# Kernel tuning notes

Hardware: AMD Instinct MI355X
Metric: run time of the kernel (lower is better)

The kernel has to match this reference:

```python
import jax, jax.numpy as jnp
import numpy as np

D_OUT = 512          # full_tensor_dims[0]
VIEW_DIMS = (512, 512, 512)
RANK = 32
BATCH = 4096


def _xavier(key, shape):
    # xavier-style init: scale by sqrt(2 / (fan_in + fan_out)) over first/last dims
    fan_in, fan_out = shape[0] * shape[1], shape[2]
    scale = jnp.sqrt(2.0 / (fan_in + fan_out)).astype(jnp.float32)
    return jax.random.normal(key, shape, dtype=jnp.float32) * scale


def setup_inputs() -> dict:
    key = jax.random.key(0)
    ks = jax.random.split(key, 8)
    X0 = jax.random.normal(ks[0], (VIEW_DIMS[0], BATCH), dtype=jnp.float32)
    X1 = jax.random.normal(ks[1], (VIEW_DIMS[1], BATCH), dtype=jnp.float32)
    X2 = jax.random.normal(ks[2], (VIEW_DIMS[2], BATCH), dtype=jnp.float32)
    # TT cores: rank chain [1, 32, 32, 32, 1]
    core0 = _xavier(ks[3], (1, D_OUT, RANK))            # [1, d_out, r1]
    core1 = _xavier(ks[4], (RANK, VIEW_DIMS[0], RANK))  # [r1, d1, r2]
    core2 = _xavier(ks[5], (RANK, VIEW_DIMS[1], RANK))  # [r2, d2, r3]
    core3 = _xavier(ks[6], (RANK, VIEW_DIMS[2], 1))     # [r3, d3, 1]
    return {"X0": X0, "X1": X1, "X2": X2,
            "core0": core0, "core1": core1, "core2": core2, "core3": core3}


def reference(X0, X1, X2, core0, core1, core2, core3):
    # Batched equivalent of the per-sample Python loop in TensorTrain.forward.
    # For each view j: M_j[n] = mode_dot(core_{j+1}^T_{0,2,1}, X_j[:, n], mode=2)
    #   == einsum('adb,dn->nab'), shape [B, r_{j+1}, r_{j+2}]
    Xs = (X0, X1, X2)
    chain_cores = (core1, core2, core3)
    Ms = [jnp.einsum('adb,dn->nab', c, x) for c, x in zip(chain_cores, Xs)]
    # Chain of per-sample matmuls: z = M_0 @ M_1 @ M_2 -> [B, r1, 1]
    acc = Ms[0]
    for M in Ms[1:]:
        acc = jnp.einsum('nab,nbc->nac', acc, M)
    # Z[:, n] = mode_dot(core0, z[:, 0], mode=2)[0, :]
    Z = jnp.einsum('oda,na->dn', core0, acc[:, :, 0])  # [d_out, B]
    return Z


if __name__ == '__main__':
    out = reference(**setup_inputs())
    print(out.shape)
```

## Files before the change

### kernel.cpp

```cpp
#include <hip/hip_runtime.h>

#define D 512
#define B 4096
#define R 32
#define AB 1024

typedef unsigned short ushort_t;
typedef __attribute__((ext_vector_type(8))) short bf16x8;
typedef __attribute__((ext_vector_type(4))) float f32x4;

__device__ __forceinline__ ushort_t f2bf(float f) {
  uint32_t u = __builtin_bit_cast(uint32_t, f);
  u = (u + 0x7FFFu + ((u >> 16) & 1u)) >> 16;
  return (ushort_t)u;
}
__device__ __forceinline__ float bf2f(ushort_t h) {
  uint32_t u = ((uint32_t)h) << 16;
  return __builtin_bit_cast(float, u);
}
__device__ __forceinline__ void gload_lds16(const void* g, void* lds) {
  __builtin_amdgcn_global_load_lds(
      (const __attribute__((address_space(1))) unsigned int*)g,
      (__attribute__((address_space(3))) unsigned int*)lds, 16, 0, 0);
}

__global__ __launch_bounds__(256) void pack_cores(
    const float* __restrict__ c1, const float* __restrict__ c2,
    ushort_t* __restrict__ Apack)
{
  __shared__ ushort_t T[R][D + 8];
  const int ja = blockIdx.x, j = ja >> 5, a = ja & 31;
  const float* __restrict__ c = j ? c2 : c1;
  const int tid = threadIdx.x;
#pragma unroll
  for (int i = 0; i < 64; ++i) {
    int e = i * 256 + tid;
    T[e & 31][e >> 5] = f2bf(c[(size_t)a * (D * R) + e]);
  }
  __syncthreads();
#pragma unroll
  for (int i = 0; i < 8; ++i) {
    int ch = i * 256 + tid;
    int b = ch >> 6, off = (ch & 63) * 8;
    ushort_t v[8];
#pragma unroll
    for (int q = 0; q < 8; ++q) v[q] = T[b][off + q];
    *(bf16x8*)&Apack[((size_t)j * AB + a * 32 + b) * D + off] = *(bf16x8*)v;
  }
}

__global__ __launch_bounds__(256) void transpose_x(
    const float* __restrict__ X0, const float* __restrict__ X1,
    ushort_t* __restrict__ Xt)
{
  __shared__ float T[64][65];
  const int j = blockIdx.z;
  const float* __restrict__ X = j ? X1 : X0;
  ushort_t* __restrict__ O = Xt + (size_t)j * B * D;
  const int n0 = blockIdx.x * 64, d0 = blockIdx.y * 64;
  const int tid = threadIdx.x;
#pragma unroll
  for (int i = 0; i < 16; ++i) {
    int e = i * 256 + tid;
    T[e >> 6][e & 63] = X[(size_t)(d0 + (e >> 6)) * B + n0 + (e & 63)];
  }
  __syncthreads();
#pragma unroll
  for (int i = 0; i < 2; ++i) {
    int ch = i * 256 + tid;
    int nr = ch >> 3, dc = (ch & 7) * 8;
    ushort_t v[8];
#pragma unroll
    for (int q = 0; q < 8; ++q) v[q] = f2bf(T[dc + q][nr]);
    *(bf16x8*)&O[(size_t)(n0 + nr) * D + d0 + dc] = *(bf16x8*)v;
  }
}

__global__ __launch_bounds__(256) void gemm_mfma(
    const ushort_t* __restrict__ Apack, const ushort_t* __restrict__ Xt,
    ushort_t* __restrict__ Mt)
{
  __shared__ __align__(16) ushort_t smem[17408];
  ushort_t* As0 = smem;
  ushort_t* As1 = smem + 4096;
  ushort_t* Bs0 = smem + 8192;
  ushort_t* Bs1 = smem + 12288;

  const int j = blockIdx.z;
  const ushort_t* __restrict__ Ag = Xt + (size_t)j * B * D;
  const ushort_t* __restrict__ Bg = Apack + (size_t)j * AB * D;
  ushort_t* __restrict__ C = Mt + (size_t)j * B * AB;

  const int tid = threadIdx.x;
  const int lane = tid & 63, wid = tid >> 6;
  const int wr = wid >> 1, wc = wid & 1;
  const int nBase = blockIdx.y * 128;
  const int rBase = blockIdx.x * 128;

  const int t0 = wid * 128 + lane, t1 = t0 + 64;
  const int r0 = t0 >> 2, u0 = (t0 & 3) ^ (r0 & 3);
  const int r1 = t1 >> 2, u1 = (t1 & 3) ^ (r1 & 3);
  const ushort_t* gA0 = Ag + (size_t)(nBase + r0) * D + u0 * 8;
  const ushort_t* gA1 = Ag + (size_t)(nBase + r1) * D + u1 * 8;
  const ushort_t* gB0 = Bg + (size_t)(rBase + r0) * D + u0 * 8;
  const ushort_t* gB1 = Bg + (size_t)(rBase + r1) * D + u1 * 8;
  const int lq0 = wid * 1024, lq1 = wid * 1024 + 512;

  int aoff[4], boff[4];
#pragma unroll
  for (int m = 0; m < 4; ++m) {
    int row = wr * 64 + m * 16 + (lane & 15);
    aoff[m] = row * 32 + (((lane >> 4) ^ (row & 3)) * 8);
  }
#pragma unroll
  for (int n = 0; n < 4; ++n) {
    int col = wc * 64 + n * 16 + (lane & 15);
    boff[n] = col * 32 + (((lane >> 4) ^ (col & 3)) * 8);
  }

  f32x4 acc[4][4] = {};

  auto stage = [&](ushort_t* Asb, ushort_t* Bsb, int k0) {
    gload_lds16(gA0 + k0, Asb + lq0);
    gload_lds16(gA1 + k0, Asb + lq1);
    gload_lds16(gB0 + k0, Bsb + lq0);
    gload_lds16(gB1 + k0, Bsb + lq1);
  };
  auto compute = [&](const ushort_t* Asb, const ushort_t* Bsb) {
    bf16x8 a[4], b[4];
#pragma unroll
    for (int m = 0; m < 4; ++m) a[m] = *(const bf16x8*)&Asb[aoff[m]];
#pragma unroll
    for (int n = 0; n < 4; ++n) b[n] = *(const bf16x8*)&Bsb[boff[n]];
#pragma unroll
    for (int m = 0; m < 4; ++m)
#pragma unroll
      for (int n = 0; n < 4; ++n)
        acc[m][n] = __builtin_amdgcn_mfma_f32_16x16x32_bf16(a[m], b[n], acc[m][n], 0, 0, 0);
  };

  stage(As0, Bs0, 0);
  __syncthreads();
#pragma unroll 1
  for (int kp = 0; kp < 8; ++kp) {
    stage(As1, Bs1, kp * 64 + 32);
    compute(As0, Bs0);
    __syncthreads();
    if (kp < 7) stage(As0, Bs0, kp * 64 + 64);
    compute(As1, Bs1);
    __syncthreads();
  }

#define TLD 136
  ushort_t* T = smem;
  const int qn = (lane >> 4) << 2;
#pragma unroll
  for (int m = 0; m < 4; ++m)
#pragma unroll
    for (int nn = 0; nn < 4; ++nn) {
      int nl = wr * 64 + m * 16 + qn;
      int rl = wc * 64 + nn * 16 + (lane & 15);
#pragma unroll
      for (int r = 0; r < 4; ++r)
        T[(nl + r) * TLD + rl] = f2bf(acc[m][nn][r]);
    }
  __syncthreads();
#pragma unroll
  for (int i = 0; i < 8; ++i) {
    int nl = i * 16 + (tid >> 4);
    int rl = (tid & 15) * 8;
    bf16x8 v = *(const bf16x8*)&T[nl * TLD + rl];
    *(bf16x8*)&C[(size_t)(nBase + nl) * AB + rBase + rl] = v;
  }
}

__global__ __launch_bounds__(256) void m2_kernel(
    const float* __restrict__ X2, const float* __restrict__ core3,
    float* __restrict__ m2t)
{
  const int tid = threadIdx.x;
  const int n0 = blockIdx.x * 32;
  const int n = tid & 31, q = tid >> 5;
  float acc[4] = {};
  for (int d = 0; d < D; ++d) {
    float x = X2[(size_t)d * B + n0 + n];
#pragma unroll
    for (int cc = 0; cc < 4; ++cc)
      acc[cc] += core3[(q * 4 + cc) * D + d] * x;
  }
#pragma unroll
  for (int cc = 0; cc < 4; ++cc)
    m2t[(size_t)(n0 + n) * R + q * 4 + cc] = acc[cc];
}

__global__ __launch_bounds__(256) void chain_kernel(
    const ushort_t* __restrict__ Mt, const float* __restrict__ m2t,
    float* __restrict__ zt)
{
  __shared__ float ts[4][R];
  const int tid = threadIdx.x;
  const int lane = tid & 63, w = tid >> 6;
  const int h = lane & 1, g = lane >> 1;
  const ushort_t* __restrict__ Mt0 = Mt;
  const ushort_t* __restrict__ Mt1 = Mt + (size_t)B * AB;
  const int nb = blockIdx.x * 8 + w * 2;

#pragma unroll
  for (int s = 0; s < 2; ++s) {
    const int n = nb + s;
    const size_t rowbase = (size_t)n * AB + lane * 16;

    float4 m2v[4];
#pragma unroll
    for (int q = 0; q < 4; ++q)
      m2v[q] = *(const float4*)&m2t[(size_t)n * R + h * 16 + q * 4];

    bf16x8 m1a = *(const bf16x8*)&Mt1[rowbase];
    bf16x8 m1b = *(const bf16x8*)&Mt1[rowbase + 8];
    bf16x8 m0a = *(const bf16x8*)&Mt0[rowbase];
    bf16x8 m0b = *(const bf16x8*)&Mt0[rowbase + 8];

    float m2f[16] = {m2v[0].x, m2v[0].y, m2v[0].z, m2v[0].w,
                     m2v[1].x, m2v[1].y, m2v[1].z, m2v[1].w,
                     m2v[2].x, m2v[2].y, m2v[2].z, m2v[2].w,
                     m2v[3].x, m2v[3].y, m2v[3].z, m2v[3].w};
    float pt = 0.f;
#pragma unroll
    for (int k = 0; k < 8; ++k) pt += bf2f((ushort_t)m1a[k]) * m2f[k];
#pragma unroll
    for (int k = 0; k < 8; ++k) pt += bf2f((ushort_t)m1b[k]) * m2f[8 + k];
    pt += __shfl_xor(pt, 1, 64);
    if (h == 0) ts[w][g] = pt;

    float pz = 0.f;
#pragma unroll
    for (int k = 0; k < 8; ++k) pz += bf2f((ushort_t)m0a[k]) * ts[w][h * 16 + k];
#pragma unroll
    for (int k = 0; k < 8; ++k) pz += bf2f((ushort_t)m0b[k]) * ts[w][h * 16 + 8 + k];
    pz += __shfl_xor(pz, 1, 64);
    if (h == 0) zt[(size_t)n * R + g] = pz;
  }
}

__global__ __launch_bounds__(256) void zgemm(
    const float* __restrict__ zt, const float* __restrict__ core0,
    float* __restrict__ out)
{
  __shared__ float c0s[64][R];
  __shared__ float zs[R][132];
  const int n0 = blockIdx.x * 128, d0 = blockIdx.y * 64;
  const int tid = threadIdx.x;
#pragma unroll
  for (int i = 0; i < 4; ++i) {
    int ch = i * 256 + tid;
    int nr = ch >> 3, a4 = (ch & 7) * 4;
    float4 v = *(const float4*)&zt[(size_t)(n0 + nr) * R + a4];
    zs[a4 + 0][nr] = v.x; zs[a4 + 1][nr] = v.y;
    zs[a4 + 2][nr] = v.z; zs[a4 + 3][nr] = v.w;
  }
#pragma unroll
  for (int i = 0; i < 2; ++i) {
    int ch = i * 256 + tid;
    int rr = ch >> 3, off = (ch & 7) * 4;
    *(float4*)&c0s[rr][off] = *(const float4*)&core0[(size_t)(d0 + rr) * R + off];
  }
  __syncthreads();
  const int tx = tid & 31, ty = tid >> 5;
  float acc[8][4] = {};
  for (int k = 0; k < R; ++k) {
    float4 z4 = *(const float4*)&zs[k][tx * 4];
    float zz[4] = {z4.x, z4.y, z4.z, z4.w};
#pragma unroll
    for (int i = 0; i < 8; ++i) {
      float cv = c0s[ty * 8 + i][k];
#pragma unroll
      for (int jj = 0; jj < 4; ++jj) acc[i][jj] += cv * zz[jj];
    }
  }
#pragma unroll
  for (int i = 0; i < 8; ++i) {
    float4 o = {acc[i][0], acc[i][1], acc[i][2], acc[i][3]};
    *(float4*)&out[(size_t)(d0 + ty * 8 + i) * B + n0 + tx * 4] = o;
  }
}

extern "C" void kernel_launch(void* const* d_in, const int* in_sizes, int n_in,
                              void* d_out, int out_size, void* d_ws, size_t ws_size,
                              hipStream_t stream)
{
  const float* X0    = (const float*)d_in[0];
  const float* X1    = (const float*)d_in[1];
  const float* X2    = (const float*)d_in[2];
  const float* core0 = (const float*)d_in[3];
  const float* core1 = (const float*)d_in[4];
  const float* core2 = (const float*)d_in[5];
  const float* core3 = (const float*)d_in[6];
  float* out = (float*)d_out;

  char* ws = (char*)d_ws;
  ushort_t* Apack = (ushort_t*)(ws);
  ushort_t* Xt    = (ushort_t*)(ws + (2u << 20));
  ushort_t* Mt    = (ushort_t*)(ws + (10u << 20));
  float*    m2t   = (float*)   (ws + (26u << 20));
  float*    zt    = (float*)   (ws + (27u << 20));

  hipLaunchKernelGGL(pack_cores, dim3(64), dim3(256), 0, stream, core1, core2, Apack);
  hipLaunchKernelGGL(transpose_x, dim3(64, 8, 2), dim3(256), 0, stream, X0, X1, Xt);
  hipLaunchKernelGGL(gemm_mfma, dim3(8, 32, 2), dim3(256), 0, stream, Apack, Xt, Mt);
  hipLaunchKernelGGL(m2_kernel, dim3(128), dim3(256), 0, stream, X2, core3, m2t);
  hipLaunchKernelGGL(chain_kernel, dim3(512), dim3(256), 0, stream, Mt, m2t, zt);
  hipLaunchKernelGGL(zgemm, dim3(32, 8), dim3(256), 0, stream, zt, core0, out);
}
```

Measured before the change: 140.0 us.

## Merge prep kernels and route core3 contraction through the MFMA GEMM

Folds pack_cores and transpose_x into a single prep kernel that also transposes X2 and packs core3 into a zero-padded 128-row bf16 matrix. The scalar fp32 m2_kernel is removed, and its contraction runs as 32 extra blocks in the flat-indexed MFMA GEMM, with results stored as bf16 in Mt2. This cuts two launches and replaces a slow serial dot-product loop with tensor-core work. In exchange it adds an X2 transpose pass, wastes compute on 96 padded zero rows, and lowers the m2 path precision to bf16.

```diff
diff --git a/kernel.cpp b/kernel.cpp
--- a/kernel.cpp
+++ b/kernel.cpp
@@ -24,61 +24,79 @@
       (__attribute__((address_space(3))) unsigned int*)lds, 16, 0, 0);
 }
 
-__global__ __launch_bounds__(256) void pack_cores(
-    const float* __restrict__ c1, const float* __restrict__ c2,
-    ushort_t* __restrict__ Apack)
-{
-  __shared__ ushort_t T[R][D + 8];
-  const int ja = blockIdx.x, j = ja >> 5, a = ja & 31;
-  const float* __restrict__ c = j ? c2 : c1;
-  const int tid = threadIdx.x;
-#pragma unroll
-  for (int i = 0; i < 64; ++i) {
-    int e = i * 256 + tid;
-    T[e & 31][e >> 5] = f2bf(c[(size_t)a * (D * R) + e]);
-  }
-  __syncthreads();
-#pragma unroll
-  for (int i = 0; i < 8; ++i) {
-    int ch = i * 256 + tid;
-    int b = ch >> 6, off = (ch & 63) * 8;
-    ushort_t v[8];
-#pragma unroll
-    for (int q = 0; q < 8; ++q) v[q] = T[b][off + q];
-    *(bf16x8*)&Apack[((size_t)j * AB + a * 32 + b) * D + off] = *(bf16x8*)v;
-  }
-}
-
-__global__ __launch_bounds__(256) void transpose_x(
+__global__ __launch_bounds__(256) void prep(
     const float* __restrict__ X0, const float* __restrict__ X1,
-    ushort_t* __restrict__ Xt)
-{
-  __shared__ float T[64][65];
-  const int j = blockIdx.z;
-  const float* __restrict__ X = j ? X1 : X0;
-  ushort_t* __restrict__ O = Xt + (size_t)j * B * D;
-  const int n0 = blockIdx.x * 64, d0 = blockIdx.y * 64;
-  const int tid = threadIdx.x;
-#pragma unroll
-  for (int i = 0; i < 16; ++i) {
-    int e = i * 256 + tid;
-    T[e >> 6][e & 63] = X[(size_t)(d0 + (e >> 6)) * B + n0 + (e & 63)];
-  }
-  __syncthreads();
-#pragma unroll
-  for (int i = 0; i < 2; ++i) {
-    int ch = i * 256 + tid;
-    int nr = ch >> 3, dc = (ch & 7) * 8;
-    ushort_t v[8];
-#pragma unroll
-    for (int q = 0; q < 8; ++q) v[q] = f2bf(T[dc + q][nr]);
-    *(bf16x8*)&O[(size_t)(n0 + nr) * D + d0 + dc] = *(bf16x8*)v;
+    const float* __restrict__ X2, const float* __restrict__ c1,
+    const float* __restrict__ c2, const float* __restrict__ c3,
+    ushort_t* __restrict__ Xt, ushort_t* __restrict__ Apack,
+    ushort_t* __restrict__ Apack3)
+{
+  __shared__ __align__(16) char smem[33280];
+  const int bid = blockIdx.x, tid = threadIdx.x;
+
+  if (bid < 1536) {
+    float (*T)[65] = (float(*)[65])smem;
+    const int v = bid / 512, tile = bid % 512;
+    const float* __restrict__ X = (v == 0) ? X0 : ((v == 1) ? X1 : X2);
+    ushort_t* __restrict__ O = Xt + (size_t)v * B * D;
+    const int n0 = (tile & 63) * 64, d0 = (tile >> 6) * 64;
+#pragma unroll
+    for (int i = 0; i < 16; ++i) {
+      int e = i * 256 + tid;
+      T[e >> 6][e & 63] = X[(size_t)(d0 + (e >> 6)) * B + n0 + (e & 63)];
+    }
+    __syncthreads();
+#pragma unroll
+    for (int i = 0; i < 2; ++i) {
+      int ch = i * 256 + tid;
+      int nr = ch >> 3, dc = (ch & 7) * 8;
+      ushort_t w[8];
+#pragma unroll
+      for (int q = 0; q < 8; ++q) w[q] = f2bf(T[dc + q][nr]);
+      *(bf16x8*)&O[(size_t)(n0 + nr) * D + d0 + dc] = *(bf16x8*)w;
+    }
+  } else if (bid < 1600) {
+    ushort_t (*T)[D + 8] = (ushort_t(*)[D + 8])smem;
+    const int ja = bid - 1536, j = ja >> 5, a = ja & 31;
+    const float* __restrict__ c = j ? c2 : c1;
+#pragma unroll
+    for (int i = 0; i < 64; ++i) {
+      int e = i * 256 + tid;
+      T[e & 31][e >> 5] = f2bf(c[(size_t)a * (D * R) + e]);
+    }
+    __syncthreads();
+#pragma unroll
+    for (int i = 0; i < 8; ++i) {
+      int ch = i * 256 + tid;
+      int b = ch >> 6, off = (ch & 63) * 8;
+      ushort_t w[8];
+#pragma unroll
+      for (int q = 0; q < 8; ++q) w[q] = T[b][off + q];
+      *(bf16x8*)&Apack[((size_t)j * AB + a * 32 + b) * D + off] = *(bf16x8*)w;
+    }
+  } else {
+    const int r0 = (bid - 1600) * 16;
+#pragma unroll
+    for (int i = 0; i < 4; ++i) {
+      int ch = i * 256 + tid;
+      int rr = r0 + (ch >> 6), off = (ch & 63) * 8;
+      ushort_t w[8];
+      if (rr < R) {
+#pragma unroll
+        for (int q = 0; q < 8; ++q) w[q] = f2bf(c3[(size_t)rr * D + off + q]);
+      } else {
+#pragma unroll
+        for (int q = 0; q < 8; ++q) w[q] = 0;
+      }
+      *(bf16x8*)&Apack3[(size_t)rr * D + off] = *(bf16x8*)w;
+    }
   }
 }
 
 __global__ __launch_bounds__(256) void gemm_mfma(
-    const ushort_t* __restrict__ Apack, const ushort_t* __restrict__ Xt,
-    ushort_t* __restrict__ Mt)
+    const ushort_t* __restrict__ Apack, const ushort_t* __restrict__ Apack3,
+    const ushort_t* __restrict__ Xt, ushort_t* __restrict__ Mt,
+    ushort_t* __restrict__ Mt2)
 {
   __shared__ __align__(16) ushort_t smem[17408];
   ushort_t* As0 = smem;
@@ -86,16 +104,27 @@
   ushort_t* Bs0 = smem + 8192;
   ushort_t* Bs1 = smem + 12288;
 
-  const int j = blockIdx.z;
-  const ushort_t* __restrict__ Ag = Xt + (size_t)j * B * D;
-  const ushort_t* __restrict__ Bg = Apack + (size_t)j * AB * D;
-  ushort_t* __restrict__ C = Mt + (size_t)j * B * AB;
+  const int bid = blockIdx.x;
+  int j, rb, nb, ldc;
+  const ushort_t *Ag, *Bg;
+  ushort_t* C;
+  if (bid < 512) {
+    j = bid >> 8; int w = bid & 255; rb = w >> 5; nb = w & 31;
+    Ag = Xt + (size_t)j * B * D;
+    Bg = Apack + (size_t)j * AB * D;
+    C  = Mt + (size_t)j * B * AB;  ldc = AB;
+  } else {
+    j = 2; rb = 0; nb = bid - 512;
+    Ag = Xt + (size_t)2 * B * D;
+    Bg = Apack3;
+    C  = Mt2;  ldc = 128;
+  }
 
   const int tid = threadIdx.x;
   const int lane = tid & 63, wid = tid >> 6;
   const int wr = wid >> 1, wc = wid & 1;
-  const int nBase = blockIdx.y * 128;
-  const int rBase = blockIdx.x * 128;
+  const int nBase = nb * 128;
+  const int rBase = rb * 128;
 
   const int t0 = wid * 128 + lane, t1 = t0 + 64;
   const int r0 = t0 >> 2, u0 = (t0 & 3) ^ (r0 & 3);
@@ -170,31 +199,12 @@
     int nl = i * 16 + (tid >> 4);
     int rl = (tid & 15) * 8;
     bf16x8 v = *(const bf16x8*)&T[nl * TLD + rl];
-    *(bf16x8*)&C[(size_t)(nBase + nl) * AB + rBase + rl] = v;
-  }
-}
-
-__global__ __launch_bounds__(256) void m2_kernel(
-    const float* __restrict__ X2, const float* __restrict__ core3,
-    float* __restrict__ m2t)
-{
-  const int tid = threadIdx.x;
-  const int n0 = blockIdx.x * 32;
-  const int n = tid & 31, q = tid >> 5;
-  float acc[4] = {};
-  for (int d = 0; d < D; ++d) {
-    float x = X2[(size_t)d * B + n0 + n];
-#pragma unroll
-    for (int cc = 0; cc < 4; ++cc)
-      acc[cc] += core3[(q * 4 + cc) * D + d] * x;
-  }
-#pragma unroll
-  for (int cc = 0; cc < 4; ++cc)
-    m2t[(size_t)(n0 + n) * R + q * 4 + cc] = acc[cc];
+    *(bf16x8*)&C[(size_t)(nBase + nl) * ldc + rBase + rl] = v;
+  }
 }
 
 __global__ __launch_bounds__(256) void chain_kernel(
-    const ushort_t* __restrict__ Mt, const float* __restrict__ m2t,
+    const ushort_t* __restrict__ Mt, const ushort_t* __restrict__ Mt2,
     float* __restrict__ zt)
 {
   __shared__ float ts[4][R];
@@ -210,25 +220,19 @@
     const int n = nb + s;
     const size_t rowbase = (size_t)n * AB + lane * 16;
 
-    float4 m2v[4];
-#pragma unroll
-    for (int q = 0; q < 4; ++q)
-      m2v[q] = *(const float4*)&m2t[(size_t)n * R + h * 16 + q * 4];
+    bf16x8 m2a = *(const bf16x8*)&Mt2[(size_t)n * 128 + h * 16];
+    bf16x8 m2b = *(const bf16x8*)&Mt2[(size_t)n * 128 + h * 16 + 8];
 
     bf16x8 m1a = *(const bf16x8*)&Mt1[rowbase];
     bf16x8 m1b = *(const bf16x8*)&Mt1[rowbase + 8];
     bf16x8 m0a = *(const bf16x8*)&Mt0[rowbase];
     bf16x8 m0b = *(const bf16x8*)&Mt0[rowbase + 8];
 
-    float m2f[16] = {m2v[0].x, m2v[0].y, m2v[0].z, m2v[0].w,
-                     m2v[1].x, m2v[1].y, m2v[1].z, m2v[1].w,
-                     m2v[2].x, m2v[2].y, m2v[2].z, m2v[2].w,
-                     m2v[3].x, m2v[3].y, m2v[3].z, m2v[3].w};
     float pt = 0.f;
 #pragma unroll
-    for (int k = 0; k < 8; ++k) pt += bf2f((ushort_t)m1a[k]) * m2f[k];
-#pragma unroll
-    for (int k = 0; k < 8; ++k) pt += bf2f((ushort_t)m1b[k]) * m2f[8 + k];
+    for (int k = 0; k < 8; ++k) pt += bf2f((ushort_t)m1a[k]) * bf2f((ushort_t)m2a[k]);
+#pragma unroll
+    for (int k = 0; k < 8; ++k) pt += bf2f((ushort_t)m1b[k]) * bf2f((ushort_t)m2b[k]);
     pt += __shfl_xor(pt, 1, 64);
     if (h == 0) ts[w][g] = pt;
 
@@ -298,16 +302,17 @@
   float* out = (float*)d_out;
 
   char* ws = (char*)d_ws;
-  ushort_t* Apack = (ushort_t*)(ws);
-  ushort_t* Xt    = (ushort_t*)(ws + (2u << 20));
-  ushort_t* Mt    = (ushort_t*)(ws + (10u << 20));
-  float*    m2t   = (float*)   (ws + (26u << 20));
-  float*    zt    = (float*)   (ws + (27u << 20));
-
-  hipLaunchKernelGGL(pack_cores, dim3(64), dim3(256), 0, stream, core1, core2, Apack);
-  hipLaunchKernelGGL(transpose_x, dim3(64, 8, 2), dim3(256), 0, stream, X0, X1, Xt);
-  hipLaunchKernelGGL(gemm_mfma, dim3(8, 32, 2), dim3(256), 0, stream, Apack, Xt, Mt);
-  hipLaunchKernelGGL(m2_kernel, dim3(128), dim3(256), 0, stream, X2, core3, m2t);
-  hipLaunchKernelGGL(chain_kernel, dim3(512), dim3(256), 0, stream, Mt, m2t, zt);
+  ushort_t* Apack  = (ushort_t*)(ws);
+  ushort_t* Apack3 = (ushort_t*)(ws + (2u  << 20));
+  ushort_t* Xt     = (ushort_t*)(ws + (4u  << 20));
+  ushort_t* Mt     = (ushort_t*)(ws + (16u << 20));
+  ushort_t* Mt2    = (ushort_t*)(ws + (32u << 20));
+  float*    zt     = (float*)   (ws + (33u << 20));
+
+  hipLaunchKernelGGL(prep, dim3(1608), dim3(256), 0, stream,
+                     X0, X1, X2, core1, core2, core3, Xt, Apack, Apack3);
+  hipLaunchKernelGGL(gemm_mfma, dim3(544), dim3(256), 0, stream,
+                     Apack, Apack3, Xt, Mt, Mt2);
+  hipLaunchKernelGGL(chain_kernel, dim3(512), dim3(256), 0, stream, Mt, Mt2, zt);
   hipLaunchKernelGGL(zgemm, dim3(32, 8), dim3(256), 0, stream, zt, core0, out);
 }
```

After: 112.3 us. 1.25x faster.
